# Performance work log

Hardware: AMD Instinct MI355X
Metric: run time of the kernel (lower is better)

The kernel has to match this reference:

```python
import jax, jax.numpy as jnp
import numpy as np

B, S, H = 2, 2048, 1024
NH, HD = 16, 64  # num heads, head dim
EPS = 1e-12


def setup_inputs() -> dict:
    key = jax.random.key(0)
    ks = jax.random.split(key, 10)
    sc = 1.0 / np.sqrt(H)
    return {
        "hidden_states": jax.random.normal(ks[0], (B, S, H), jnp.float32),
        "Wq": jax.random.normal(ks[1], (H, H), jnp.float32) * sc,
        "bq": jnp.zeros((H,), jnp.float32),
        "Wk": jax.random.normal(ks[2], (H, H), jnp.float32) * sc,
        "bk": jnp.zeros((H,), jnp.float32),
        "Wv": jax.random.normal(ks[3], (H, H), jnp.float32) * sc,
        "bv": jnp.zeros((H,), jnp.float32),
        "Wo": jax.random.normal(ks[4], (H, H), jnp.float32) * sc,
        "bo": jnp.zeros((H,), jnp.float32),
        "ln_g": jnp.ones((H,), jnp.float32),
        "ln_b": jnp.zeros((H,), jnp.float32),
    }


def reference(hidden_states, Wq, bq, Wk, bk, Wv, bv, Wo, bo, ln_g, ln_b):
    x = hidden_states  # [B,S,H]
    def split_heads(t):
        return t.reshape(B, S, NH, HD).transpose(0, 2, 1, 3)  # [B,NH,S,HD]
    q = split_heads(x @ Wq.T + bq)
    k = split_heads(x @ Wk.T + bk)
    v = split_heads(x @ Wv.T + bv)
    scores = jnp.einsum("bhqd,bhkd->bhqk", q, k) / np.sqrt(HD)
    causal = jnp.tril(jnp.ones((S, S), bool))  # [S,S]
    scores = jnp.where(causal[None, None], scores, -jnp.inf)
    probs = jax.nn.softmax(scores, axis=-1)
    ctx = jnp.einsum("bhqk,bhkd->bhqd", probs, v)
    ctx = ctx.transpose(0, 2, 1, 3).reshape(B, S, H)
    attn_out = ctx @ Wo.T + bo
    y = attn_out + x
    mu = jnp.mean(y, axis=-1, keepdims=True)
    var = jnp.mean((y - mu) ** 2, axis=-1, keepdims=True)
    return (y - mu) / jnp.sqrt(var + EPS) * ln_g + ln_b
```

## Files before the change

### kernel.cpp

```cpp
#include <hip/hip_runtime.h>

#define B_  2
#define S_  2048
#define H_  1024
#define NH_ 16
#define HD_ 64
#define M_  (B_*S_)

typedef __attribute__((ext_vector_type(8))) __bf16 bf16x8;
typedef __attribute__((ext_vector_type(4))) float  f32x4;
typedef __attribute__((ext_vector_type(8))) unsigned short us8;
typedef __attribute__((ext_vector_type(4))) float  fl4;

#define GL16(g, l) __builtin_amdgcn_global_load_lds( \
    (const __attribute__((address_space(1))) unsigned int*)(g), \
    (__attribute__((address_space(3))) unsigned int*)(l), 16, 0, 0)

__device__ __forceinline__ unsigned short f2bf(float f) {
    unsigned int u = __float_as_uint(f);
    u += 0x7fffu + ((u >> 16) & 1u);
    return (unsigned short)(u >> 16);
}

__global__ __launch_bounds__(256) void cast_kernel(
    const float* __restrict__ x,
    const float* __restrict__ wq, const float* __restrict__ wk,
    const float* __restrict__ wv, const float* __restrict__ wo,
    unsigned short* __restrict__ xb, unsigned short* __restrict__ wb) {
    size_t t  = (size_t)blockIdx.x * 256 + threadIdx.x;
    size_t e0 = t * 4;
    const size_t XN = (size_t)M_ * H_;
    const float* src;
    unsigned short* dst;
    if (e0 < XN) { src = x + e0; dst = xb + e0; }
    else {
        size_t j = e0 - XN;
        int w = (int)(j >> 20);
        size_t off = j & ((1u << 20) - 1);
        const float* wp = (w == 0) ? wq : (w == 1) ? wk : (w == 2) ? wv : wo;
        src = wp + off; dst = wb + j;
    }
    fl4 v = *(const fl4*)src;
    ushort4 o;
    o.x = f2bf(v.x); o.y = f2bf(v.y); o.z = f2bf(v.z); o.w = f2bf(v.w);
    *(ushort4*)dst = o;
}

__global__ __launch_bounds__(256) void gemm_qkv(
    const unsigned short* __restrict__ xb, const unsigned short* __restrict__ wb,
    const float* __restrict__ bq, const float* __restrict__ bk,
    const float* __restrict__ bv,
    unsigned short* __restrict__ qb, unsigned short* __restrict__ kbuf,
    unsigned short* __restrict__ vT) {
    __shared__ __align__(16) unsigned short As[128 * 64];
    __shared__ __align__(16) unsigned short Bs[128 * 64];
    const int z = blockIdx.z;
    const unsigned short* W = wb + ((size_t)z << 20);
    const int m0 = blockIdx.x * 128, n0 = blockIdx.y * 128;
    const int t = threadIdx.x, lane = t & 63, w = t >> 6;
    const int wm = w >> 1, wn = w & 1, quad = lane >> 4, l16 = lane & 15;
    const int srow = w * 32 + (lane >> 3);
    const int scol = (lane & 7) * 8;
    const unsigned short* ga = xb + (size_t)(m0 + srow) * H_ + scol;
    const unsigned short* gb = W  + (size_t)(n0 + srow) * H_ + scol;

    f32x4 acc[4][4] = {};
    for (int k0 = 0; k0 < H_; k0 += 64) {
        __syncthreads();
#pragma unroll
        for (int j = 0; j < 4; j++) {
            GL16(ga + (size_t)(j * 8) * H_ + k0, &As[(w * 32 + j * 8) * 64]);
            GL16(gb + (size_t)(j * 8) * H_ + k0, &Bs[(w * 32 + j * 8) * 64]);
        }
        __syncthreads();
#pragma unroll
        for (int kk = 0; kk < 64; kk += 32) {
            bf16x8 af[4], bfr[4];
#pragma unroll
            for (int i = 0; i < 4; i++)
                af[i]  = *(const bf16x8*)&As[(wm * 64 + i * 16 + l16) * 64 + kk + quad * 8];
#pragma unroll
            for (int i = 0; i < 4; i++)
                bfr[i] = *(const bf16x8*)&Bs[(wn * 64 + i * 16 + l16) * 64 + kk + quad * 8];
#pragma unroll
            for (int mi = 0; mi < 4; mi++)
#pragma unroll
                for (int ni = 0; ni < 4; ni++)
                    acc[mi][ni] = __builtin_amdgcn_mfma_f32_16x16x32_bf16(
                        af[mi], bfr[ni], acc[mi][ni], 0, 0, 0);
        }
    }
    const float* bias = (z == 0) ? bq : (z == 1) ? bk : bv;
    if (z == 2) {
#pragma unroll
        for (int mi = 0; mi < 4; mi++) {
#pragma unroll
            for (int ni = 0; ni < 4; ni++) {
                int col  = n0 + wn * 64 + ni * 16 + l16;
                float bval = bias[col];
                int row0 = m0 + wm * 64 + mi * 16 + quad * 4;
                int bb = row0 >> 11, s0 = row0 & 2047;
                ushort4 pk;
                pk.x = f2bf(acc[mi][ni][0] + bval);
                pk.y = f2bf(acc[mi][ni][1] + bval);
                pk.z = f2bf(acc[mi][ni][2] + bval);
                pk.w = f2bf(acc[mi][ni][3] + bval);
                *(ushort4*)&vT[((size_t)bb * NH_ * HD_ + col) * S_ + s0] = pk;
            }
        }
    } else {
        unsigned short* out = (z == 0) ? qb : kbuf;
        const float qs = (z == 0) ? 0.18033688f : 1.0f;
#pragma unroll
        for (int mi = 0; mi < 4; mi++) {
#pragma unroll
            for (int ni = 0; ni < 4; ni++) {
                int col = n0 + wn * 64 + ni * 16 + l16;
                float bval = bias[col];
#pragma unroll
                for (int r = 0; r < 4; r++) {
                    int row = m0 + wm * 64 + mi * 16 + quad * 4 + r;
                    out[(size_t)row * H_ + col] = f2bf((acc[mi][ni][r] + bval) * qs);
                }
            }
        }
    }
}

__global__ __launch_bounds__(256) void gemm_out(
    const unsigned short* __restrict__ ctxb, const unsigned short* __restrict__ wob,
    const float* __restrict__ bo, const float* __restrict__ x,
    float* __restrict__ y) {
    __shared__ __align__(16) unsigned short As[128 * 64];
    __shared__ __align__(16) unsigned short Bs[64 * 64];
    const int m0 = blockIdx.x * 128, n0 = blockIdx.y * 64;
    const int t = threadIdx.x, lane = t & 63, w = t >> 6;
    const int quad = lane >> 4, l16 = lane & 15;
    const int l8r = lane >> 3, l8c = (lane & 7) * 8;
    const unsigned short* ga = ctxb + (size_t)(m0 + w * 32 + l8r) * H_ + l8c;
    const unsigned short* gb = wob  + (size_t)(n0 + w * 16 + l8r) * H_ + l8c;

    f32x4 acc[2][4] = {};
    for (int k0 = 0; k0 < H_; k0 += 64) {
        __syncthreads();
#pragma unroll
        for (int j = 0; j < 4; j++)
            GL16(ga + (size_t)(j * 8) * H_ + k0, &As[(w * 32 + j * 8) * 64]);
#pragma unroll
        for (int j = 0; j < 2; j++)
            GL16(gb + (size_t)(j * 8) * H_ + k0, &Bs[(w * 16 + j * 8) * 64]);
        __syncthreads();
#pragma unroll
        for (int kk = 0; kk < 64; kk += 32) {
            bf16x8 af[2], bfr[4];
#pragma unroll
            for (int i = 0; i < 2; i++)
                af[i]  = *(const bf16x8*)&As[(w * 32 + i * 16 + l16) * 64 + kk + quad * 8];
#pragma unroll
            for (int i = 0; i < 4; i++)
                bfr[i] = *(const bf16x8*)&Bs[(i * 16 + l16) * 64 + kk + quad * 8];
#pragma unroll
            for (int mi = 0; mi < 2; mi++)
#pragma unroll
                for (int ni = 0; ni < 4; ni++)
                    acc[mi][ni] = __builtin_amdgcn_mfma_f32_16x16x32_bf16(
                        af[mi], bfr[ni], acc[mi][ni], 0, 0, 0);
        }
    }
#pragma unroll
    for (int mi = 0; mi < 2; mi++) {
#pragma unroll
        for (int ni = 0; ni < 4; ni++) {
            int col = n0 + ni * 16 + l16;
            float bval = bo[col];
#pragma unroll
            for (int r = 0; r < 4; r++) {
                size_t idx = (size_t)(m0 + w * 32 + mi * 16 + quad * 4 + r) * H_ + col;
                y[idx] = acc[mi][ni][r] + bval + x[idx];
            }
        }
    }
}

__global__ __launch_bounds__(512, 4) void attn_kernel(
    const unsigned short* __restrict__ qb, const unsigned short* __restrict__ kb,
    const unsigned short* __restrict__ vT, unsigned short* __restrict__ ctxb) {
    __shared__ __align__(16) unsigned short Ks[2][64 * 72];
    __shared__ __align__(16) unsigned short Vt[2][64 * 72];
    __shared__ __align__(16) unsigned short Ps[128 * 76];
    const int flat = blockIdx.x;
    const int xcd = flat & 7, slot = flat >> 3;
    const int bh  = xcd * 4 + (slot >> 3);
    const int j   = slot & 7;
    const int b = bh >> 4, h = bh & 15;
    const int t = threadIdx.x, lane = t & 63, wid = t >> 6;
    const int grp = wid >> 2, wid4 = wid & 3;
    const int quad = lane >> 4, l16 = lane & 15;
    const int sr8 = t >> 3, sc8 = (t & 7) * 8;
    const size_t headoff = (size_t)h * HD_;
    const unsigned short* vtb = vT + ((size_t)(b * NH_ + h) * HD_) * S_;

    const int p   = j * 2 + grp;
    const int qt1 = p, qt2 = 31 - p;
    const int q01 = qt1 * 64, q02 = qt2 * 64;

    const size_t qr1 = (size_t)(b * S_ + q01 + wid4 * 16 + l16);
    const size_t qr2 = (size_t)(b * S_ + q02 + wid4 * 16 + l16);
    bf16x8 q1a = *(const bf16x8*)(qb + qr1 * H_ + headoff + quad * 8);
    bf16x8 q1b = *(const bf16x8*)(qb + qr1 * H_ + headoff + 32 + quad * 8);
    bf16x8 q2a = *(const bf16x8*)(qb + qr2 * H_ + headoff + quad * 8);
    bf16x8 q2b = *(const bf16x8*)(qb + qr2 * H_ + headoff + 32 + quad * 8);

    float m1 = -1e30f, l1 = 0.f, m2 = -1e30f, l2 = 0.f;
    f32x4 o1[4] = {}, o2[4] = {};

    const unsigned short* kptr = kb  + (size_t)(b * S_ + sr8) * H_ + headoff + sc8;
    const unsigned short* vptr = vtb + (size_t)sr8 * S_ + sc8;
    us8 nk = *(const us8*)kptr;
    us8 nv = *(const us8*)vptr;
    *(us8*)&Ks[0][sr8 * 72 + sc8] = nk;
    *(us8*)&Vt[0][sr8 * 72 + sc8] = nv;
    __syncthreads();

    for (int s = 0; s < 32; s++) {
        const int buf = s & 1;
        const bool pf = (s < 31);
        if (pf) {
            kptr += (size_t)64 * H_;
            vptr += 64;
            nk = *(const us8*)kptr;
            nv = *(const us8*)vptr;
        }
#pragma unroll
        for (int tile = 0; tile < 2; tile++) {
            const int  qt  = tile ? qt2 : qt1;
            if (s > qt) continue;
            const bf16x8 qa = tile ? q2a : q1a;
            const bf16x8 qb_ = tile ? q2b : q1b;
            f32x4 sacc[4] = {};
#pragma unroll
            for (int kk = 0; kk < 64; kk += 32) {
                bf16x8 bqf = (kk == 0) ? qa : qb_;
#pragma unroll
                for (int nt = 0; nt < 4; nt++) {
                    bf16x8 ak = *(const bf16x8*)&Ks[buf][(nt * 16 + l16) * 72 + kk + quad * 8];
                    sacc[nt] = __builtin_amdgcn_mfma_f32_16x16x32_bf16(ak, bqf, sacc[nt], 0, 0, 0);
                }
            }
            if (s == qt) {
#pragma unroll
                for (int nt = 0; nt < 4; nt++) {
#pragma unroll
                    for (int r = 0; r < 4; r++) {
                        int key = nt * 16 + quad * 4 + r;
                        if (key > wid4 * 16 + l16) sacc[nt][r] = -1e30f;
                    }
                }
            }
            float mx = sacc[0][0];
#pragma unroll
            for (int nt = 0; nt < 4; nt++)
#pragma unroll
                for (int r = 0; r < 4; r++) mx = fmaxf(mx, sacc[nt][r]);
            mx = fmaxf(mx, __shfl_xor(mx, 16));
            mx = fmaxf(mx, __shfl_xor(mx, 32));
            float m_old = tile ? m2 : m1;
            float m_new = fmaxf(m_old, mx);
            float alpha = exp2f(m_old - m_new);
            float ss = 0.f;
#pragma unroll
            for (int nt = 0; nt < 4; nt++) {
                ushort4 pk;
                float p0 = exp2f(sacc[nt][0] - m_new);
                float p1 = exp2f(sacc[nt][1] - m_new);
                float p2 = exp2f(sacc[nt][2] - m_new);
                float p3 = exp2f(sacc[nt][3] - m_new);
                ss += (p0 + p1) + (p2 + p3);
                pk.x = (unsigned short)(__float_as_uint(p0) >> 16);
                pk.y = (unsigned short)(__float_as_uint(p1) >> 16);
                pk.z = (unsigned short)(__float_as_uint(p2) >> 16);
                pk.w = (unsigned short)(__float_as_uint(p3) >> 16);
                *(ushort4*)&Ps[(wid * 16 + l16) * 76 + nt * 16 + quad * 4] = pk;
            }
            ss += __shfl_xor(ss, 16);
            ss += __shfl_xor(ss, 32);
            if (tile) { l2 = l2 * alpha + ss; m2 = m_new; }
            else      { l1 = l1 * alpha + ss; m1 = m_new; }
            f32x4* oo = tile ? o2 : o1;
#pragma unroll
            for (int dt = 0; dt < 4; dt++)
#pragma unroll
                for (int r = 0; r < 4; r++) oo[dt][r] *= alpha;
            __threadfence_block();
#pragma unroll
            for (int kk = 0; kk < 64; kk += 32) {
                bf16x8 pfr = *(const bf16x8*)&Ps[(wid * 16 + l16) * 76 + kk + quad * 8];
#pragma unroll
                for (int dt = 0; dt < 4; dt++) {
                    bf16x8 vf = *(const bf16x8*)&Vt[buf][(dt * 16 + l16) * 72 + kk + quad * 8];
                    oo[dt] = __builtin_amdgcn_mfma_f32_16x16x32_bf16(vf, pfr, oo[dt], 0, 0, 0);
                }
            }
        }
        if (pf) {
            *(us8*)&Ks[buf ^ 1][sr8 * 72 + sc8] = nk;
            *(us8*)&Vt[buf ^ 1][sr8 * 72 + sc8] = nv;
            __syncthreads();
        }
    }
#pragma unroll
    for (int tile = 0; tile < 2; tile++) {
        const int q0 = tile ? q02 : q01;
        const float inv = 1.0f / (tile ? l2 : l1);
        const f32x4* oo = tile ? o2 : o1;
        size_t row = (size_t)(b * S_ + q0 + wid4 * 16 + l16);
#pragma unroll
        for (int dt = 0; dt < 4; dt++) {
            ushort4 pk;
            pk.x = f2bf(oo[dt][0] * inv);
            pk.y = f2bf(oo[dt][1] * inv);
            pk.z = f2bf(oo[dt][2] * inv);
            pk.w = f2bf(oo[dt][3] * inv);
            *(ushort4*)&ctxb[row * H_ + headoff + dt * 16 + quad * 4] = pk;
        }
    }
}

__global__ __launch_bounds__(256) void ln_kernel(
    const float* __restrict__ y, const float* __restrict__ g,
    const float* __restrict__ bta, float* __restrict__ out) {
    __shared__ float red[8];
    const int row = blockIdx.x, t = threadIdx.x;
    fl4 v = *(const fl4*)(y + (size_t)row * H_ + t * 4);
    float s  = v.x + v.y + v.z + v.w;
    float sq = v.x * v.x + v.y * v.y + v.z * v.z + v.w * v.w;
    for (int m = 1; m < 64; m <<= 1) { s += __shfl_xor(s, m); sq += __shfl_xor(sq, m); }
    const int wid = t >> 6, lane = t & 63;
    if (lane == 0) { red[wid * 2] = s; red[wid * 2 + 1] = sq; }
    __syncthreads();
    s  = red[0] + red[2] + red[4] + red[6];
    sq = red[1] + red[3] + red[5] + red[7];
    float mu   = s * (1.0f / H_);
    float var  = sq * (1.0f / H_) - mu * mu;
    float rstd = rsqrtf(fmaxf(var, 0.f) + 1e-12f);
    fl4 gg = *(const fl4*)(g + t * 4);
    fl4 bb = *(const fl4*)(bta + t * 4);
    fl4 o;
    o.x = (v.x - mu) * rstd * gg.x + bb.x;
    o.y = (v.y - mu) * rstd * gg.y + bb.y;
    o.z = (v.z - mu) * rstd * gg.z + bb.z;
    o.w = (v.w - mu) * rstd * gg.w + bb.w;
    *(fl4*)(out + (size_t)row * H_ + t * 4) = o;
}

extern "C" void kernel_launch(void* const* d_in, const int* in_sizes, int n_in,
                              void* d_out, int out_size, void* d_ws, size_t ws_size,
                              hipStream_t stream) {
    const float* x  = (const float*)d_in[0];
    const float* Wq = (const float*)d_in[1];
    const float* bq = (const float*)d_in[2];
    const float* Wk = (const float*)d_in[3];
    const float* bk = (const float*)d_in[4];
    const float* Wv = (const float*)d_in[5];
    const float* bv = (const float*)d_in[6];
    const float* Wo = (const float*)d_in[7];
    const float* bo = (const float*)d_in[8];
    const float* lg = (const float*)d_in[9];
    const float* lb = (const float*)d_in[10];
    float* out = (float*)d_out;

    const size_t MEG = 1024u * 1024u;
    unsigned short* ws16 = (unsigned short*)d_ws;
    unsigned short* xb   = ws16;
    unsigned short* wb   = ws16 + 4 * MEG;
    unsigned short* qb   = ws16 + 8 * MEG;
    unsigned short* kb   = ws16 + 12 * MEG;
    unsigned short* vT   = ws16 + 16 * MEG;
    unsigned short* ctxb = ws16 + 20 * MEG;
    float* y = (float*)(ws16 + 24 * MEG);

    cast_kernel<<<8192, 256, 0, stream>>>(x, Wq, Wk, Wv, Wo, xb, wb);
    gemm_qkv<<<dim3(32, 8, 3), 256, 0, stream>>>(xb, wb, bq, bk, bv, qb, kb, vT);
    attn_kernel<<<dim3(256), 512, 0, stream>>>(qb, kb, vT, ctxb);
    gemm_out<<<dim3(32, 16), 256, 0, stream>>>(ctxb, wb + 3 * MEG, bo, x, y);
    ln_kernel<<<4096, 256, 0, stream>>>(y, lg, lb, out);
}
```

Before: 217.1 us.

## Register-prefetch GEMM tiles with padded LDS and 512-thread blocks

```diff
diff --git a/kernel.cpp b/kernel.cpp
--- a/kernel.cpp
+++ b/kernel.cpp
@@ -11,10 +11,6 @@
 typedef __attribute__((ext_vector_type(4))) float  f32x4;
 typedef __attribute__((ext_vector_type(8))) unsigned short us8;
 typedef __attribute__((ext_vector_type(4))) float  fl4;
-
-#define GL16(g, l) __builtin_amdgcn_global_load_lds( \
-    (const __attribute__((address_space(1))) unsigned int*)(g), \
-    (__attribute__((address_space(3))) unsigned int*)(l), 16, 0, 0)
 
 __device__ __forceinline__ unsigned short f2bf(float f) {
     unsigned int u = __float_as_uint(f);
@@ -46,46 +42,51 @@
     *(ushort4*)dst = o;
 }
 
-__global__ __launch_bounds__(256) void gemm_qkv(
+__global__ __launch_bounds__(512) void gemm_qkv(
     const unsigned short* __restrict__ xb, const unsigned short* __restrict__ wb,
     const float* __restrict__ bq, const float* __restrict__ bk,
     const float* __restrict__ bv,
     unsigned short* __restrict__ qb, unsigned short* __restrict__ kbuf,
     unsigned short* __restrict__ vT) {
-    __shared__ __align__(16) unsigned short As[128 * 64];
-    __shared__ __align__(16) unsigned short Bs[128 * 64];
+    __shared__ __align__(16) unsigned short As[128 * 72];
+    __shared__ __align__(16) unsigned short Bs[128 * 72];
     const int z = blockIdx.z;
     const unsigned short* W = wb + ((size_t)z << 20);
     const int m0 = blockIdx.x * 128, n0 = blockIdx.y * 128;
     const int t = threadIdx.x, lane = t & 63, w = t >> 6;
-    const int wm = w >> 1, wn = w & 1, quad = lane >> 4, l16 = lane & 15;
-    const int srow = w * 32 + (lane >> 3);
-    const int scol = (lane & 7) * 8;
-    const unsigned short* ga = xb + (size_t)(m0 + srow) * H_ + scol;
-    const unsigned short* gb = W  + (size_t)(n0 + srow) * H_ + scol;
-
-    f32x4 acc[4][4] = {};
+    const int wm = w >> 2, wn = w & 3;
+    const int quad = lane >> 4, l16 = lane & 15;
+    const int sr = t >> 2, sc = (t & 3) * 16;
+    const unsigned short* ga = xb + (size_t)(m0 + sr) * H_ + sc;
+    const unsigned short* gb = W  + (size_t)(n0 + sr) * H_ + sc;
+
+    us8 a0 = *(const us8*)(ga),     a1 = *(const us8*)(ga + 8);
+    us8 b0 = *(const us8*)(gb),     b1 = *(const us8*)(gb + 8);
+
+    f32x4 acc[4][2] = {};
     for (int k0 = 0; k0 < H_; k0 += 64) {
+        if (k0) __syncthreads();
+        *(us8*)&As[sr * 72 + sc]     = a0;  *(us8*)&As[sr * 72 + sc + 8] = a1;
+        *(us8*)&Bs[sr * 72 + sc]     = b0;  *(us8*)&Bs[sr * 72 + sc + 8] = b1;
         __syncthreads();
-#pragma unroll
-        for (int j = 0; j < 4; j++) {
-            GL16(ga + (size_t)(j * 8) * H_ + k0, &As[(w * 32 + j * 8) * 64]);
-            GL16(gb + (size_t)(j * 8) * H_ + k0, &Bs[(w * 32 + j * 8) * 64]);
-        }
-        __syncthreads();
+        if (k0 + 64 < H_) {
+            ga += 64; gb += 64;
+            a0 = *(const us8*)(ga);  a1 = *(const us8*)(ga + 8);
+            b0 = *(const us8*)(gb);  b1 = *(const us8*)(gb + 8);
+        }
 #pragma unroll
         for (int kk = 0; kk < 64; kk += 32) {
-            bf16x8 af[4], bfr[4];
+            bf16x8 af[4], bfr[2];
 #pragma unroll
             for (int i = 0; i < 4; i++)
-                af[i]  = *(const bf16x8*)&As[(wm * 64 + i * 16 + l16) * 64 + kk + quad * 8];
-#pragma unroll
-            for (int i = 0; i < 4; i++)
-                bfr[i] = *(const bf16x8*)&Bs[(wn * 64 + i * 16 + l16) * 64 + kk + quad * 8];
+                af[i]  = *(const bf16x8*)&As[(wm * 64 + i * 16 + l16) * 72 + kk + quad * 8];
+#pragma unroll
+            for (int jn = 0; jn < 2; jn++)
+                bfr[jn] = *(const bf16x8*)&Bs[(wn * 32 + jn * 16 + l16) * 72 + kk + quad * 8];
 #pragma unroll
             for (int mi = 0; mi < 4; mi++)
 #pragma unroll
-                for (int ni = 0; ni < 4; ni++)
+                for (int ni = 0; ni < 2; ni++)
                     acc[mi][ni] = __builtin_amdgcn_mfma_f32_16x16x32_bf16(
                         af[mi], bfr[ni], acc[mi][ni], 0, 0, 0);
         }
@@ -95,8 +96,8 @@
 #pragma unroll
         for (int mi = 0; mi < 4; mi++) {
 #pragma unroll
-            for (int ni = 0; ni < 4; ni++) {
-                int col  = n0 + wn * 64 + ni * 16 + l16;
+            for (int ni = 0; ni < 2; ni++) {
+                int col  = n0 + wn * 32 + ni * 16 + l16;
                 float bval = bias[col];
                 int row0 = m0 + wm * 64 + mi * 16 + quad * 4;
                 int bb = row0 >> 11, s0 = row0 & 2047;
@@ -114,8 +115,8 @@
 #pragma unroll
         for (int mi = 0; mi < 4; mi++) {
 #pragma unroll
-            for (int ni = 0; ni < 4; ni++) {
-                int col = n0 + wn * 64 + ni * 16 + l16;
+            for (int ni = 0; ni < 2; ni++) {
+                int col = n0 + wn * 32 + ni * 16 + l16;
                 float bval = bias[col];
 #pragma unroll
                 for (int r = 0; r < 4; r++) {
@@ -127,55 +128,60 @@
     }
 }
 
-__global__ __launch_bounds__(256) void gemm_out(
+__global__ __launch_bounds__(512) void gemm_out(
     const unsigned short* __restrict__ ctxb, const unsigned short* __restrict__ wob,
     const float* __restrict__ bo, const float* __restrict__ x,
     float* __restrict__ y) {
-    __shared__ __align__(16) unsigned short As[128 * 64];
-    __shared__ __align__(16) unsigned short Bs[64 * 64];
-    const int m0 = blockIdx.x * 128, n0 = blockIdx.y * 64;
+    __shared__ __align__(16) unsigned short As[128 * 72];
+    __shared__ __align__(16) unsigned short Bs[128 * 72];
+    const int m0 = blockIdx.x * 128, n0 = blockIdx.y * 128;
     const int t = threadIdx.x, lane = t & 63, w = t >> 6;
+    const int wm = w >> 2, wn = w & 3;
     const int quad = lane >> 4, l16 = lane & 15;
-    const int l8r = lane >> 3, l8c = (lane & 7) * 8;
-    const unsigned short* ga = ctxb + (size_t)(m0 + w * 32 + l8r) * H_ + l8c;
-    const unsigned short* gb = wob  + (size_t)(n0 + w * 16 + l8r) * H_ + l8c;
-
-    f32x4 acc[2][4] = {};
+    const int sr = t >> 2, sc = (t & 3) * 16;
+    const unsigned short* ga = ctxb + (size_t)(m0 + sr) * H_ + sc;
+    const unsigned short* gb = wob  + (size_t)(n0 + sr) * H_ + sc;
+
+    us8 a0 = *(const us8*)(ga),     a1 = *(const us8*)(ga + 8);
+    us8 b0 = *(const us8*)(gb),     b1 = *(const us8*)(gb + 8);
+
+    f32x4 acc[4][2] = {};
     for (int k0 = 0; k0 < H_; k0 += 64) {
+        if (k0) __syncthreads();
+        *(us8*)&As[sr * 72 + sc]     = a0;  *(us8*)&As[sr * 72 + sc + 8] = a1;
+        *(us8*)&Bs[sr * 72 + sc]     = b0;  *(us8*)&Bs[sr * 72 + sc + 8] = b1;
         __syncthreads();
-#pragma unroll
-        for (int j = 0; j < 4; j++)
-            GL16(ga + (size_t)(j * 8) * H_ + k0, &As[(w * 32 + j * 8) * 64]);
-#pragma unroll
-        for (int j = 0; j < 2; j++)
-            GL16(gb + (size_t)(j * 8) * H_ + k0, &Bs[(w * 16 + j * 8) * 64]);
-        __syncthreads();
+        if (k0 + 64 < H_) {
+            ga += 64; gb += 64;
+            a0 = *(const us8*)(ga);  a1 = *(const us8*)(ga + 8);
+            b0 = *(const us8*)(gb);  b1 = *(const us8*)(gb + 8);
+        }
 #pragma unroll
         for (int kk = 0; kk < 64; kk += 32) {
-            bf16x8 af[2], bfr[4];
-#pragma unroll
-            for (int i = 0; i < 2; i++)
-                af[i]  = *(const bf16x8*)&As[(w * 32 + i * 16 + l16) * 64 + kk + quad * 8];
+            bf16x8 af[4], bfr[2];
 #pragma unroll
             for (int i = 0; i < 4; i++)
-                bfr[i] = *(const bf16x8*)&Bs[(i * 16 + l16) * 64 + kk + quad * 8];
-#pragma unroll
-            for (int mi = 0; mi < 2; mi++)
-#pragma unroll
-                for (int ni = 0; ni < 4; ni++)
+                af[i]  = *(const bf16x8*)&As[(wm * 64 + i * 16 + l16) * 72 + kk + quad * 8];
+#pragma unroll
+            for (int jn = 0; jn < 2; jn++)
+                bfr[jn] = *(const bf16x8*)&Bs[(wn * 32 + jn * 16 + l16) * 72 + kk + quad * 8];
+#pragma unroll
+            for (int mi = 0; mi < 4; mi++)
+#pragma unroll
+                for (int ni = 0; ni < 2; ni++)
                     acc[mi][ni] = __builtin_amdgcn_mfma_f32_16x16x32_bf16(
                         af[mi], bfr[ni], acc[mi][ni], 0, 0, 0);
         }
     }
 #pragma unroll
-    for (int mi = 0; mi < 2; mi++) {
-#pragma unroll
-        for (int ni = 0; ni < 4; ni++) {
-            int col = n0 + ni * 16 + l16;
+    for (int mi = 0; mi < 4; mi++) {
+#pragma unroll
+        for (int ni = 0; ni < 2; ni++) {
+            int col = n0 + wn * 32 + ni * 16 + l16;
             float bval = bo[col];
 #pragma unroll
             for (int r = 0; r < 4; r++) {
-                size_t idx = (size_t)(m0 + w * 32 + mi * 16 + quad * 4 + r) * H_ + col;
+                size_t idx = (size_t)(m0 + wm * 64 + mi * 16 + quad * 4 + r) * H_ + col;
                 y[idx] = acc[mi][ni][r] + bval + x[idx];
             }
         }
@@ -380,8 +386,8 @@
     float* y = (float*)(ws16 + 24 * MEG);
 
     cast_kernel<<<8192, 256, 0, stream>>>(x, Wq, Wk, Wv, Wo, xb, wb);
-    gemm_qkv<<<dim3(32, 8, 3), 256, 0, stream>>>(xb, wb, bq, bk, bv, qb, kb, vT);
+    gemm_qkv<<<dim3(32, 8, 3), 512, 0, stream>>>(xb, wb, bq, bk, bv, qb, kb, vT);
     attn_kernel<<<dim3(256), 512, 0, stream>>>(qb, kb, vT, ctxb);
-    gemm_out<<<dim3(32, 16), 256, 0, stream>>>(ctxb, wb + 3 * MEG, bo, x, y);
+    gemm_out<<<dim3(32, 8), 512, 0, stream>>>(ctxb, wb + 3 * MEG, bo, x, y);
     ln_kernel<<<4096, 256, 0, stream>>>(y, lg, lb, out);
 }
```

Result: faster. 200.3 us (-7.8%).
